# Optimization experiments

Hardware: AMD Instinct MI355X
Metric: run time of the kernel (lower is better)

Reference implementation:

```python
import jax, jax.numpy as jnp
import numpy as np

ALPHA, BETA, GAMMA, SMOOTH = 0.3, 0.7, 1.33, 1e-06
LOVASZ_WEIGHT = 0.2


def setup_inputs() -> dict:
    key = jax.random.key(0)
    k1, k2 = jax.random.split(key)
    logits = jax.random.normal(k1, (32, 1, 512, 512), dtype=jnp.float32)
    targets = jax.random.randint(k2, (32, 1, 512, 512), 0, 2, dtype=jnp.int32)
    return {"logits": logits, "targets": targets}


def _lovasz_hinge_flat(log_flat, lab_flat):
    # log_flat, lab_flat: [P]
    signs = 2.0 * lab_flat - 1.0
    errors = 1.0 - log_flat * signs
    perm = jnp.argsort(-errors)  # descending sort by errors
    errors_sorted = errors[perm]
    labels_sorted = lab_flat[perm]
    p = labels_sorted.sum()
    n = labels_sorted.shape[0] - p
    intersection = p - jnp.cumsum(labels_sorted)
    union = p + jnp.cumsum(1.0 - labels_sorted)
    jaccard = 1.0 - intersection / union
    jaccard_diff = jnp.concatenate([jaccard[:1], jaccard[1:] - jaccard[:-1]])
    grad = jnp.where(n > 0, jaccard_diff, jaccard)
    return jnp.dot(jax.nn.relu(errors_sorted), grad)


def reference(logits, targets):
    t = targets.astype(jnp.float32)
    B = logits.shape[0]
    # Focal-Tversky term
    p = jax.nn.sigmoid(logits).reshape(B, -1)
    tf = t.reshape(B, -1)
    tp = jnp.sum(p * tf, axis=1)
    fn = jnp.sum((1.0 - p) * tf, axis=1)
    fp = jnp.sum(p * (1.0 - tf), axis=1)
    tversky = (tp + SMOOTH) / (tp + ALPHA * fn + BETA * fp + SMOOTH)
    ft = jnp.mean((1.0 - tversky) ** GAMMA)
    # Lovasz hinge, per image (vmapped instead of python loop)
    log_flat = logits.reshape(B, -1)
    lab_flat = tf
    lov = jnp.mean(jax.vmap(_lovasz_hinge_flat)(log_flat, lab_flat))
    return ft + LOVASZ_WEIGHT * lov
```

## Files before the change

### kernel.cpp

```cpp
#include <hip/hip_runtime.h>

#define NIMG 32
#define PIMG (512 * 512)
#define BINS 512
#define BPI 64
#define K1_THREADS 256
#define CHUNK (PIMG / BPI)
#define PER_T (CHUNK / K1_THREADS)
#define NB4 (PER_T / 4)
#define K2_THREADS 256
#define POS_PER_T (BINS / K2_THREADS)
#define FIXED_SCALE 17592186044416.0

__device__ __forceinline__ float sigmoidf_(float x) {
    return __builtin_amdgcn_rcpf(1.0f + __expf(-x));
}

#define OFF_GTV   (NIMG * BPI * BINS * 4)
#define OFF_GACC  (OFF_GTV + NIMG * BPI * 16)

__global__ __launch_bounds__(K1_THREADS, 8) void k1_hist(
    const float* __restrict__ logits, const int* __restrict__ targets,
    unsigned* __restrict__ gpart, float4* __restrict__ gtv,
    unsigned long long* __restrict__ gacc) {
    __shared__ unsigned hcq[BINS];
    __shared__ float red[12];

    const int tid = threadIdx.x;
    const int img = blockIdx.x >> 6;
    const int blk = blockIdx.x & 63;

    if (blockIdx.x == 0 && tid == 0) { gacc[0] = 0ull; gacc[1] = 0ull; }

#pragma unroll
    for (int i = 0; i < BINS / K1_THREADS; ++i) hcq[tid + i * K1_THREADS] = 0u;
    __syncthreads();

    const long long base = (long long)img * PIMG + (long long)blk * CHUNK;
    const float4* lg4 = reinterpret_cast<const float4*>(logits + base);
    const int4* tg4 = reinterpret_cast<const int4*>(targets + base);

    float4 x4[NB4];
    int4 t4[NB4];
#pragma unroll
    for (int it = 0; it < NB4; ++it) {
        x4[it] = lg4[it * K1_THREADS + tid];
        t4[it] = tg4[it * K1_THREADS + tid];
    }

    float tp = 0.0f, Ssum = 0.0f;
    unsigned pc = 0;

#pragma unroll
    for (int it = 0; it < NB4; ++it) {
#pragma unroll
        for (int j = 0; j < 4; ++j) {
            float x = (&x4[it].x)[j];
            int t = (&t4[it].x)[j];
            float s = sigmoidf_(x);
            Ssum += s;
            if (t) { tp += s; pc++; }
            float e = t ? (1.0f - x) : (1.0f + x);
            if (e >= 0.0f) {
                int b = (int)(e * ((float)BINS / 8.0f));
                if (b > BINS - 1) b = BINS - 1;
                atomicAdd(&hcq[b], 0x10000u + (unsigned)t);
            }
        }
    }
    __syncthreads();

    reinterpret_cast<uint2*>(gpart + (size_t)blockIdx.x * BINS)[tid] =
        reinterpret_cast<const uint2*>(hcq)[tid];

    unsigned pcu = pc;
#pragma unroll
    for (int off = 32; off > 0; off >>= 1) {
        tp += __shfl_down(tp, off);
        Ssum += __shfl_down(Ssum, off);
        pcu += __shfl_down(pcu, off);
    }
    const int lane = tid & 63, w = tid >> 6;
    if (lane == 0) { red[w * 3] = tp; red[w * 3 + 1] = Ssum; red[w * 3 + 2] = (float)pcu; }
    __syncthreads();
    if (tid == 0) {
        gtv[blockIdx.x] = make_float4(red[0] + red[3] + red[6] + red[9],
                                      red[1] + red[4] + red[7] + red[10],
                                      red[2] + red[5] + red[8] + red[11], 0.0f);
    }
}

__global__ __launch_bounds__(K2_THREADS) void k23_lovasz(
    const unsigned* __restrict__ gpart, const float4* __restrict__ gtv,
    unsigned long long* __restrict__ gacc, float* __restrict__ out) {
    const int img = blockIdx.x;
    const int t = threadIdx.x;
    const int lane = t & 63, w = t >> 6;

    __shared__ float smx[4];
    __shared__ unsigned long long wt[8];
    __shared__ double rd[4];

    unsigned c0 = 0, q0 = 0, c1 = 0, q1 = 0;
    const unsigned* basep = gpart + ((size_t)img * BPI) * BINS;
#pragma unroll 8
    for (int blk = 0; blk < BPI; ++blk) {
        const unsigned* row = basep + (size_t)blk * BINS;
        unsigned u0 = row[t];
        unsigned u1 = row[K2_THREADS + t];
        c0 += (u0 >> 16); q0 += (u0 & 0xffffu);
        c1 += (u1 >> 16); q1 += (u1 & 0xffffu);
    }
    unsigned long long own[POS_PER_T];
    own[0] = ((unsigned long long)c0 << 32) | (unsigned long long)q0;
    own[1] = ((unsigned long long)c1 << 32) | (unsigned long long)q1;

    float4 v = make_float4(0.f, 0.f, 0.f, 0.f);
    if (t < 64) v = gtv[img * BPI + t];
#pragma unroll
    for (int off = 32; off > 0; off >>= 1) {
        v.x += __shfl_down(v.x, off);
        v.y += __shfl_down(v.y, off);
        v.z += __shfl_down(v.z, off);
    }
    if (t == 0) { smx[0] = v.x; smx[1] = v.y; smx[2] = v.z; }
    __syncthreads();
    const float tpv = smx[0], Sv = smx[1];
    const long long p = (long long)(smx[2] + 0.5f);
    const long long n = (long long)PIMG - p;

    unsigned long long runHigh = 0ull;
    double lov = 0.0;
    const double wbin = 8.0 / (double)BINS;

    for (int j = POS_PER_T - 1; j >= 0; --j) {
        const unsigned long long val = own[j];
        unsigned long long incl = val;
#pragma unroll
        for (int off = 1; off < 64; off <<= 1) {
            unsigned long long o = __shfl_down(incl, off);
            if (lane + off < 64) incl += o;
        }
        const int buf = (j & 1) * 4;
        if (lane == 0) wt[buf + w] = incl;
        __syncthreads();
        unsigned long long higher = 0ull, stepTotal = 0ull;
#pragma unroll
        for (int w2 = 0; w2 < 4; ++w2) {
            unsigned long long tw = wt[buf + w2];
            stepTotal += tw;
            if (w2 > w) higher += tw;
        }
        const unsigned long long before = runHigh + higher + (incl - val);

        const long long g = (long long)(val >> 32);
        if (g) {
            const long long q = (long long)(val & 0xffffffffull);
            const long long N0 = (long long)(before >> 32);
            const long long C0 = (long long)(before & 0xffffffffull);
            const int bin = j * K2_THREADS + t;
            const double center = ((double)bin + 0.5) * wbin;
            const long long Ib = p - C0;
            const long long Ub = p + N0 - C0;
            const long long Ia = Ib - q;
            const long long Ua = Ub + g - q;
            if (n > 0) {
                double dJ;
                if (N0 == 0) {
                    dJ = 1.0 - (double)Ia / (double)Ua;
                } else {
                    const long long num = Ib * (g - q) + q * Ub;
                    dJ = (double)num / ((double)Ua * (double)Ub);
                }
                lov += center * dJ;
            } else {
                const double Jafter = 1.0 - (double)Ia / (double)Ua;
                lov += (double)g * center * Jafter;
            }
        }
        runHigh += stepTotal;
    }

#pragma unroll
    for (int off = 32; off > 0; off >>= 1) lov += __shfl_down(lov, off);
    if (lane == 0) rd[w] = lov;
    __syncthreads();
    if (t == 0) {
        const double lovt = rd[0] + rd[1] + rd[2] + rd[3];
        const float pf = (float)p;
        const float fn = pf - tpv;
        const float fp_ = Sv - tpv;
        const float tv = (tpv + 1e-6f) / (tpv + 0.3f * fn + 0.7f * fp_ + 1e-6f);
        float bse = 1.0f - tv;
        if (bse < 0.0f) bse = 0.0f;
        const double contrib = ((double)powf(bse, 1.33f) + 0.2 * lovt) / (double)NIMG;
        const long long fx = (long long)(contrib * FIXED_SCALE);
        atomicAdd(&gacc[0], (unsigned long long)fx);
        __threadfence();
        const unsigned long long done = atomicAdd(&gacc[1], 1ull);
        if (done == (unsigned long long)(NIMG - 1)) {
            const unsigned long long sum = atomicAdd(&gacc[0], 0ull);
            out[0] = (float)((double)(long long)sum / FIXED_SCALE);
        }
    }
}

extern "C" void kernel_launch(void* const* d_in, const int* in_sizes, int n_in,
                              void* d_out, int out_size, void* d_ws, size_t ws_size,
                              hipStream_t stream) {
    const float* logits = (const float*)d_in[0];
    const int* targets = (const int*)d_in[1];
    float* out = (float*)d_out;
    char* ws = (char*)d_ws;

    unsigned* gpart = (unsigned*)ws;
    float4* gtv = (float4*)(ws + OFF_GTV);
    unsigned long long* gacc = (unsigned long long*)(ws + OFF_GACC);

    k1_hist<<<NIMG * BPI, K1_THREADS, 0, stream>>>(logits, targets, gpart, gtv, gacc);
    k23_lovasz<<<NIMG, K2_THREADS, 0, stream>>>(gpart, gtv, gacc, out);
}
```

Measured before the change: 24.66 us.

## Split Lovasz histogram merge across 1024 threads with shared-memory reduction

The second kernel now uses 1024 threads per image: four groups of 256 threads each sum a quarter of the 64 partial histogram rows, and the quarter sums are then combined in shared memory. This cuts the serial load chain per thread from 64 rows to 16, which should lower the latency of the 32-block kernel that only partly fills the GPU. The scan and Jaccard part still runs on the first 256 threads only. The occupancy hint for the histogram kernel is also lowered from 8 to 4 blocks per CU, which gives the compiler a looser register budget for that kernel.

```diff
diff --git a/kernel.cpp b/kernel.cpp
--- a/kernel.cpp
+++ b/kernel.cpp
@@ -8,8 +8,8 @@
 #define CHUNK (PIMG / BPI)
 #define PER_T (CHUNK / K1_THREADS)
 #define NB4 (PER_T / 4)
-#define K2_THREADS 256
-#define POS_PER_T (BINS / K2_THREADS)
+#define K23_THREADS 1024
+#define QROWS (BPI / 4)
 #define FIXED_SCALE 17592186044416.0
 
 __device__ __forceinline__ float sigmoidf_(float x) {
@@ -19,7 +19,7 @@
 #define OFF_GTV   (NIMG * BPI * BINS * 4)
 #define OFF_GACC  (OFF_GTV + NIMG * BPI * 16)
 
-__global__ __launch_bounds__(K1_THREADS, 8) void k1_hist(
+__global__ __launch_bounds__(K1_THREADS, 4) void k1_hist(
     const float* __restrict__ logits, const int* __restrict__ targets,
     unsigned* __restrict__ gpart, float4* __restrict__ gtv,
     unsigned long long* __restrict__ gacc) {
@@ -90,41 +90,51 @@
     }
 }
 
-__global__ __launch_bounds__(K2_THREADS) void k23_lovasz(
+__global__ __launch_bounds__(K23_THREADS, 4) void k23_lovasz(
     const unsigned* __restrict__ gpart, const float4* __restrict__ gtv,
     unsigned long long* __restrict__ gacc, float* __restrict__ out) {
     const int img = blockIdx.x;
     const int t = threadIdx.x;
+    const int tq = t & 255;
+    const int qt = t >> 8;
     const int lane = t & 63, w = t >> 6;
 
+    __shared__ unsigned long long lh[4][BINS];
     __shared__ float smx[4];
     __shared__ unsigned long long wt[8];
     __shared__ double rd[4];
 
     unsigned c0 = 0, q0 = 0, c1 = 0, q1 = 0;
-    const unsigned* basep = gpart + ((size_t)img * BPI) * BINS;
-#pragma unroll 8
-    for (int blk = 0; blk < BPI; ++blk) {
-        const unsigned* row = basep + (size_t)blk * BINS;
-        unsigned u0 = row[t];
-        unsigned u1 = row[K2_THREADS + t];
+    const unsigned* basep = gpart + ((size_t)img * BPI + (size_t)qt * QROWS) * BINS;
+#pragma unroll
+    for (int k = 0; k < QROWS; ++k) {
+        const unsigned* row = basep + (size_t)k * BINS;
+        unsigned u0 = row[tq];
+        unsigned u1 = row[256 + tq];
         c0 += (u0 >> 16); q0 += (u0 & 0xffffu);
         c1 += (u1 >> 16); q1 += (u1 & 0xffffu);
     }
-    unsigned long long own[POS_PER_T];
-    own[0] = ((unsigned long long)c0 << 32) | (unsigned long long)q0;
-    own[1] = ((unsigned long long)c1 << 32) | (unsigned long long)q1;
+    lh[qt][tq]       = ((unsigned long long)c0 << 32) | (unsigned long long)q0;
+    lh[qt][256 + tq] = ((unsigned long long)c1 << 32) | (unsigned long long)q1;
 
     float4 v = make_float4(0.f, 0.f, 0.f, 0.f);
     if (t < 64) v = gtv[img * BPI + t];
-#pragma unroll
-    for (int off = 32; off > 0; off >>= 1) {
-        v.x += __shfl_down(v.x, off);
-        v.y += __shfl_down(v.y, off);
-        v.z += __shfl_down(v.z, off);
+    if (t < 64) {
+#pragma unroll
+        for (int off = 32; off > 0; off >>= 1) {
+            v.x += __shfl_down(v.x, off);
+            v.y += __shfl_down(v.y, off);
+            v.z += __shfl_down(v.z, off);
+        }
     }
     if (t == 0) { smx[0] = v.x; smx[1] = v.y; smx[2] = v.z; }
     __syncthreads();
+
+    unsigned long long own[2] = {0ull, 0ull};
+    if (t < 256) {
+        own[0] = lh[0][tq] + lh[1][tq] + lh[2][tq] + lh[3][tq];
+        own[1] = lh[0][256 + tq] + lh[1][256 + tq] + lh[2][256 + tq] + lh[3][256 + tq];
+    }
     const float tpv = smx[0], Sv = smx[1];
     const long long p = (long long)(smx[2] + 0.5f);
     const long long n = (long long)PIMG - p;
@@ -133,57 +143,64 @@
     double lov = 0.0;
     const double wbin = 8.0 / (double)BINS;
 
-    for (int j = POS_PER_T - 1; j >= 0; --j) {
-        const unsigned long long val = own[j];
-        unsigned long long incl = val;
-#pragma unroll
-        for (int off = 1; off < 64; off <<= 1) {
-            unsigned long long o = __shfl_down(incl, off);
-            if (lane + off < 64) incl += o;
-        }
-        const int buf = (j & 1) * 4;
-        if (lane == 0) wt[buf + w] = incl;
+    for (int j = 1; j >= 0; --j) {
+        unsigned long long val = 0ull, incl = 0ull;
+        if (t < 256) {
+            val = own[j];
+            incl = val;
+#pragma unroll
+            for (int off = 1; off < 64; off <<= 1) {
+                unsigned long long o = __shfl_down(incl, off);
+                if (lane + off < 64) incl += o;
+            }
+            if (lane == 0) wt[(j & 1) * 4 + w] = incl;
+        }
         __syncthreads();
-        unsigned long long higher = 0ull, stepTotal = 0ull;
-#pragma unroll
-        for (int w2 = 0; w2 < 4; ++w2) {
-            unsigned long long tw = wt[buf + w2];
-            stepTotal += tw;
-            if (w2 > w) higher += tw;
-        }
-        const unsigned long long before = runHigh + higher + (incl - val);
-
-        const long long g = (long long)(val >> 32);
-        if (g) {
-            const long long q = (long long)(val & 0xffffffffull);
-            const long long N0 = (long long)(before >> 32);
-            const long long C0 = (long long)(before & 0xffffffffull);
-            const int bin = j * K2_THREADS + t;
-            const double center = ((double)bin + 0.5) * wbin;
-            const long long Ib = p - C0;
-            const long long Ub = p + N0 - C0;
-            const long long Ia = Ib - q;
-            const long long Ua = Ub + g - q;
-            if (n > 0) {
-                double dJ;
-                if (N0 == 0) {
-                    dJ = 1.0 - (double)Ia / (double)Ua;
+        if (t < 256) {
+            const int buf = (j & 1) * 4;
+            unsigned long long higher = 0ull, stepTotal = 0ull;
+#pragma unroll
+            for (int w2 = 0; w2 < 4; ++w2) {
+                unsigned long long tw = wt[buf + w2];
+                stepTotal += tw;
+                if (w2 > w) higher += tw;
+            }
+            const unsigned long long before = runHigh + higher + (incl - val);
+
+            const long long g = (long long)(val >> 32);
+            if (g) {
+                const long long q = (long long)(val & 0xffffffffull);
+                const long long N0 = (long long)(before >> 32);
+                const long long C0 = (long long)(before & 0xffffffffull);
+                const int bin = j * 256 + tq;
+                const double center = ((double)bin + 0.5) * wbin;
+                const long long Ib = p - C0;
+                const long long Ub = p + N0 - C0;
+                const long long Ia = Ib - q;
+                const long long Ua = Ub + g - q;
+                if (n > 0) {
+                    double dJ;
+                    if (N0 == 0) {
+                        dJ = 1.0 - (double)Ia / (double)Ua;
+                    } else {
+                        const long long num = Ib * (g - q) + q * Ub;
+                        dJ = (double)num / ((double)Ua * (double)Ub);
+                    }
+                    lov += center * dJ;
                 } else {
-                    const long long num = Ib * (g - q) + q * Ub;
-                    dJ = (double)num / ((double)Ua * (double)Ub);
+                    const double Jafter = 1.0 - (double)Ia / (double)Ua;
+                    lov += (double)g * center * Jafter;
                 }
-                lov += center * dJ;
-            } else {
-                const double Jafter = 1.0 - (double)Ia / (double)Ua;
-                lov += (double)g * center * Jafter;
-            }
-        }
-        runHigh += stepTotal;
-    }
-
-#pragma unroll
-    for (int off = 32; off > 0; off >>= 1) lov += __shfl_down(lov, off);
-    if (lane == 0) rd[w] = lov;
+            }
+            runHigh += stepTotal;
+        }
+    }
+
+    if (t < 256) {
+#pragma unroll
+        for (int off = 32; off > 0; off >>= 1) lov += __shfl_down(lov, off);
+        if (lane == 0) rd[w] = lov;
+    }
     __syncthreads();
     if (t == 0) {
         const double lovt = rd[0] + rd[1] + rd[2] + rd[3];
@@ -218,5 +235,5 @@
     unsigned long long* gacc = (unsigned long long*)(ws + OFF_GACC);
 
     k1_hist<<<NIMG * BPI, K1_THREADS, 0, stream>>>(logits, targets, gpart, gtv, gacc);
-    k23_lovasz<<<NIMG, K2_THREADS, 0, stream>>>(gpart, gtv, gacc, out);
-}
+    k23_lovasz<<<NIMG, K23_THREADS, 0, stream>>>(gpart, gtv, gacc, out);
+}
```

Measured after the change: 23.53 us. 1.05x faster.

## Split per-image histogram merge across 8 blocks with last-block-done finish

Applied to the files above, without the earlier changes.

The second kernel used one block per image to sum 64 partial histograms, so only 32 blocks ran. It now launches 8 blocks per image: each block sums 8 rows, writes a partial to a new workspace buffer, and the last block to arrive (tracked by a per-image atomic counter) merges the 8 partials and runs the Lovasz scan. The first kernel also switches to nontemporal vector loads and changes its occupancy hint from 8 to 4. This adds an extra global round trip, fences and atomic counters in exchange for more parallelism in the merge stage.

```diff
diff --git a/kernel.cpp b/kernel.cpp
--- a/kernel.cpp
+++ b/kernel.cpp
@@ -8,21 +8,27 @@
 #define CHUNK (PIMG / BPI)
 #define PER_T (CHUNK / K1_THREADS)
 #define NB4 (PER_T / 4)
-#define K2_THREADS 256
-#define POS_PER_T (BINS / K2_THREADS)
+#define K23_THREADS 256
+#define OCTS 8
+#define ROWS_PER_OCT (BPI / OCTS)
 #define FIXED_SCALE 17592186044416.0
+
+typedef float fvec4 __attribute__((ext_vector_type(4)));
+typedef int ivec4 __attribute__((ext_vector_type(4)));
 
 __device__ __forceinline__ float sigmoidf_(float x) {
     return __builtin_amdgcn_rcpf(1.0f + __expf(-x));
 }
 
 #define OFF_GTV   (NIMG * BPI * BINS * 4)
-#define OFF_GACC  (OFF_GTV + NIMG * BPI * 16)
-
-__global__ __launch_bounds__(K1_THREADS, 8) void k1_hist(
+#define OFF_GH8   (OFF_GTV + NIMG * BPI * 16)
+#define OFF_GACC  (OFF_GH8 + NIMG * OCTS * BINS * 8)
+#define OFF_DONE  (OFF_GACC + 16)
+
+__global__ __launch_bounds__(K1_THREADS, 4) void k1_hist(
     const float* __restrict__ logits, const int* __restrict__ targets,
     unsigned* __restrict__ gpart, float4* __restrict__ gtv,
-    unsigned long long* __restrict__ gacc) {
+    unsigned long long* __restrict__ gacc, unsigned* __restrict__ done) {
     __shared__ unsigned hcq[BINS];
     __shared__ float red[12];
 
@@ -30,22 +36,25 @@
     const int img = blockIdx.x >> 6;
     const int blk = blockIdx.x & 63;
 
-    if (blockIdx.x == 0 && tid == 0) { gacc[0] = 0ull; gacc[1] = 0ull; }
+    if (blockIdx.x == 0) {
+        if (tid == 0) { gacc[0] = 0ull; gacc[1] = 0ull; }
+        if (tid < NIMG) done[tid] = 0u;
+    }
 
 #pragma unroll
     for (int i = 0; i < BINS / K1_THREADS; ++i) hcq[tid + i * K1_THREADS] = 0u;
     __syncthreads();
 
     const long long base = (long long)img * PIMG + (long long)blk * CHUNK;
-    const float4* lg4 = reinterpret_cast<const float4*>(logits + base);
-    const int4* tg4 = reinterpret_cast<const int4*>(targets + base);
-
-    float4 x4[NB4];
-    int4 t4[NB4];
+    const fvec4* lg4 = reinterpret_cast<const fvec4*>(logits + base);
+    const ivec4* tg4 = reinterpret_cast<const ivec4*>(targets + base);
+
+    fvec4 x4[NB4];
+    ivec4 t4[NB4];
 #pragma unroll
     for (int it = 0; it < NB4; ++it) {
-        x4[it] = lg4[it * K1_THREADS + tid];
-        t4[it] = tg4[it * K1_THREADS + tid];
+        x4[it] = __builtin_nontemporal_load(&lg4[it * K1_THREADS + tid]);
+        t4[it] = __builtin_nontemporal_load(&tg4[it * K1_THREADS + tid]);
     }
 
     float tp = 0.0f, Ssum = 0.0f;
@@ -55,8 +64,8 @@
     for (int it = 0; it < NB4; ++it) {
 #pragma unroll
         for (int j = 0; j < 4; ++j) {
-            float x = (&x4[it].x)[j];
-            int t = (&t4[it].x)[j];
+            float x = x4[it][j];
+            int t = t4[it][j];
             float s = sigmoidf_(x);
             Ssum += s;
             if (t) { tp += s; pc++; }
@@ -90,30 +99,50 @@
     }
 }
 
-__global__ __launch_bounds__(K2_THREADS) void k23_lovasz(
+__global__ __launch_bounds__(K23_THREADS, 4) void k23_lovasz(
     const unsigned* __restrict__ gpart, const float4* __restrict__ gtv,
+    unsigned long long* __restrict__ gh8, unsigned* __restrict__ done,
     unsigned long long* __restrict__ gacc, float* __restrict__ out) {
-    const int img = blockIdx.x;
+    const int img = blockIdx.x >> 3;
+    const int oct = blockIdx.x & (OCTS - 1);
     const int t = threadIdx.x;
     const int lane = t & 63, w = t >> 6;
 
+    __shared__ unsigned sdone;
     __shared__ float smx[4];
     __shared__ unsigned long long wt[8];
     __shared__ double rd[4];
 
     unsigned c0 = 0, q0 = 0, c1 = 0, q1 = 0;
-    const unsigned* basep = gpart + ((size_t)img * BPI) * BINS;
-#pragma unroll 8
-    for (int blk = 0; blk < BPI; ++blk) {
-        const unsigned* row = basep + (size_t)blk * BINS;
+    const unsigned* basep = gpart + ((size_t)img * BPI + oct * ROWS_PER_OCT) * BINS;
+#pragma unroll
+    for (int k = 0; k < ROWS_PER_OCT; ++k) {
+        const unsigned* row = basep + (size_t)k * BINS;
         unsigned u0 = row[t];
-        unsigned u1 = row[K2_THREADS + t];
+        unsigned u1 = row[256 + t];
         c0 += (u0 >> 16); q0 += (u0 & 0xffffu);
         c1 += (u1 >> 16); q1 += (u1 & 0xffffu);
     }
-    unsigned long long own[POS_PER_T];
-    own[0] = ((unsigned long long)c0 << 32) | (unsigned long long)q0;
-    own[1] = ((unsigned long long)c1 << 32) | (unsigned long long)q1;
+    unsigned long long* myp = gh8 + ((size_t)img * OCTS + oct) * BINS;
+    myp[t]       = ((unsigned long long)c0 << 32) | (unsigned long long)q0;
+    myp[256 + t] = ((unsigned long long)c1 << 32) | (unsigned long long)q1;
+
+    __threadfence();
+    __syncthreads();
+    if (t == 0)
+        sdone = __hip_atomic_fetch_add(&done[img], 1u, __ATOMIC_ACQ_REL,
+                                       __HIP_MEMORY_SCOPE_AGENT);
+    __syncthreads();
+    if (sdone != OCTS - 1) return;
+    __threadfence();
+
+    unsigned long long own[2] = {0ull, 0ull};
+    const unsigned long long* hb = gh8 + (size_t)img * OCTS * BINS;
+#pragma unroll
+    for (int o = 0; o < OCTS; ++o) {
+        own[0] += hb[(size_t)o * BINS + t];
+        own[1] += hb[(size_t)o * BINS + 256 + t];
+    }
 
     float4 v = make_float4(0.f, 0.f, 0.f, 0.f);
     if (t < 64) v = gtv[img * BPI + t];
@@ -133,7 +162,7 @@
     double lov = 0.0;
     const double wbin = 8.0 / (double)BINS;
 
-    for (int j = POS_PER_T - 1; j >= 0; --j) {
+    for (int j = 1; j >= 0; --j) {
         const unsigned long long val = own[j];
         unsigned long long incl = val;
 #pragma unroll
@@ -158,7 +187,7 @@
             const long long q = (long long)(val & 0xffffffffull);
             const long long N0 = (long long)(before >> 32);
             const long long C0 = (long long)(before & 0xffffffffull);
-            const int bin = j * K2_THREADS + t;
+            const int bin = j * 256 + t;
             const double center = ((double)bin + 0.5) * wbin;
             const long long Ib = p - C0;
             const long long Ub = p + N0 - C0;
@@ -197,8 +226,8 @@
         const long long fx = (long long)(contrib * FIXED_SCALE);
         atomicAdd(&gacc[0], (unsigned long long)fx);
         __threadfence();
-        const unsigned long long done = atomicAdd(&gacc[1], 1ull);
-        if (done == (unsigned long long)(NIMG - 1)) {
+        const unsigned long long dn = atomicAdd(&gacc[1], 1ull);
+        if (dn == (unsigned long long)(NIMG - 1)) {
             const unsigned long long sum = atomicAdd(&gacc[0], 0ull);
             out[0] = (float)((double)(long long)sum / FIXED_SCALE);
         }
@@ -215,8 +244,10 @@
 
     unsigned* gpart = (unsigned*)ws;
     float4* gtv = (float4*)(ws + OFF_GTV);
+    unsigned long long* gh8 = (unsigned long long*)(ws + OFF_GH8);
     unsigned long long* gacc = (unsigned long long*)(ws + OFF_GACC);
-
-    k1_hist<<<NIMG * BPI, K1_THREADS, 0, stream>>>(logits, targets, gpart, gtv, gacc);
-    k23_lovasz<<<NIMG, K2_THREADS, 0, stream>>>(gpart, gtv, gacc, out);
-}
+    unsigned* done = (unsigned*)(ws + OFF_DONE);
+
+    k1_hist<<<NIMG * BPI, K1_THREADS, 0, stream>>>(logits, targets, gpart, gtv, gacc, done);
+    k23_lovasz<<<NIMG * OCTS, K23_THREADS, 0, stream>>>(gpart, gtv, gh8, done, gacc, out);
+}
```

New measurement: 70.05 us. 184% more time.
